# Optimization experiments

Measured on AMD Instinct MI355X. Metric: run time of the kernel, lower is better.

Reference implementation:

```python
import jax, jax.numpy as jnp
import numpy as np

B, L = 4, 40960
C = 512
DMLP = 2048
TEMP = 1e-5
EPS = 1e-5
FACTOR = 2  # Smartpool factor at layer 4


def setup_inputs() -> dict:
    key = jax.random.key(0)
    ks = jax.random.split(key, 8)

    def w(k, shape, fan_in):
        return jax.random.normal(k, shape, jnp.float32) / np.float32(np.sqrt(fan_in))

    inp = {
        "x": jax.random.normal(ks[0], (B, 1, L), jnp.float32),
        "conv0_w": w(ks[1], (C, 1, 10), 10),   "conv0_b": jnp.zeros(C, jnp.float32),
        "conv1_w": w(ks[2], (C, C, 8), C * 8), "conv1_b": jnp.zeros(C, jnp.float32),
        "conv2_w": w(ks[3], (C, C, 4), C * 4), "conv2_b": jnp.zeros(C, jnp.float32),
        "conv3_w": w(ks[4], (C, C, 4), C * 4), "conv3_b": jnp.zeros(C, jnp.float32),
        "mlp_w1": w(ks[5], (C, DMLP), C),       "mlp_b1": jnp.zeros(DMLP, jnp.float32),
        "mlp_w2": w(ks[6], (DMLP, DMLP), DMLP), "mlp_b2": jnp.zeros(DMLP, jnp.float32),
        "mlp_w3": w(ks[7], (DMLP, 1), DMLP),    "mlp_b3": jnp.zeros(1, jnp.float32),
    }
    for i in range(5):  # ChannelNorm affine params (init: ones/zeros)
        inp[f"n{i}_w"] = jnp.ones(C, jnp.float32)
        inp[f"n{i}_b"] = jnp.zeros(C, jnp.float32)
    return inp


def _conv(x, w, b, stride, pad):
    # Conv1d with padding_mode='reflect': reflect-pad then VALID conv. x: [B,C,T]
    x = jnp.pad(x, ((0, 0), (0, 0), (pad, pad)), mode="reflect")
    y = jax.lax.conv_general_dilated(x, w, (stride,), "VALID",
                                     dimension_numbers=("NCH", "OIH", "NCH"))
    return y + b[None, :, None]


def _cnorm(x, g, b):
    # ChannelNorm: normalize over channel dim with unbiased variance (torch.var default)
    m = jnp.mean(x, axis=1, keepdims=True)
    v = jnp.var(x, axis=1, keepdims=True, ddof=1)
    return (x - m) * jax.lax.rsqrt(v + EPS) * g[None, :, None] + b[None, :, None]


def _forward(x, conv0_w, conv0_b, conv1_w, conv1_b, conv2_w, conv2_b, conv3_w, conv3_b,
             n0_w, n0_b, n1_w, n1_b, n2_w, n2_b, n3_w, n3_b, n4_w, n4_b,
             mlp_w1, mlp_b1, mlp_w2, mlp_b2, mlp_w3, mlp_b3):
    h = jax.nn.relu(_cnorm(_conv(x, conv0_w, conv0_b, 5, 3), n0_w, n0_b))
    h = jax.nn.relu(_cnorm(_conv(h, conv1_w, conv1_b, 4, 2), n1_w, n1_b))
    h = jax.nn.relu(_cnorm(_conv(h, conv2_w, conv2_b, 2, 1), n2_w, n2_b))
    h = jax.nn.relu(_cnorm(_conv(h, conv3_w, conv3_b, 2, 1), n3_w, n3_b))

    f = jnp.transpose(h, (0, 2, 1))  # [B,T,C]
    T = f.shape[1]

    # importance MLP (dropout inactive in eval), exact GELU, sigmoid head
    z = jax.nn.gelu(f @ mlp_w1 + mlp_b1, approximate=False)
    z = jax.nn.gelu(z @ mlp_w2 + mlp_b2, approximate=False)
    imp = jax.nn.sigmoid((z @ mlp_w3 + mlp_b3)[..., 0]) + TEMP          # [B,T]
    imp = imp / jnp.sum(imp, axis=1, keepdims=True) * (T / FACTOR)      # sums to T/factor

    # warp: cumsum -> ramp contributions -> 2x2 [[-1,1],[1,-1]] conv = double diff
    Tn = T // FACTOR  # == round(importance_cs[0,-1])
    cs = jnp.cumsum(imp, axis=1)                                        # [B,T]
    p = jnp.maximum(cs[:, :, None] - jnp.arange(Tn, dtype=cs.dtype)[None, None, :], 0.0)  # [B,T,Tn]
    pc = jnp.pad(p, ((0, 0), (0, 0), (0, 1)))
    d = pc[:, :, :-1] - pc[:, :, 1:]                                    # diff along new-time axis
    wmat = d - jnp.pad(d, ((0, 0), (1, 0), (0, 0)))[:, :-1, :]          # diff along old-time axis, [B,T,Tn]
    pooled = jnp.einsum("btn,btc->bnc", wmat, f)                        # interp_weights @ X

    out = jnp.transpose(pooled, (0, 2, 1))                              # [B,C,Tn]
    return jax.nn.relu(_cnorm(out, n4_w, n4_b))


def reference(x, conv0_w, conv0_b, conv1_w, conv1_b, conv2_w, conv2_b, conv3_w, conv3_b,
              n0_w, n0_b, n1_w, n1_b, n2_w, n2_b, n3_w, n3_b, n4_w, n4_b,
              mlp_w1, mlp_b1, mlp_w2, mlp_b2, mlp_w3, mlp_b3):
    return _forward(x, conv0_w, conv0_b, conv1_w, conv1_b, conv2_w, conv2_b, conv3_w, conv3_b,
                    n0_w, n0_b, n1_w, n1_b, n2_w, n2_b, n3_w, n3_b, n4_w, n4_b,
                    mlp_w1, mlp_b1, mlp_w2, mlp_b2, mlp_w3, mlp_b3)
```

## Files before the change

### kernel.cpp

```cpp
#include <hip/hip_runtime.h>
#include <hip/hip_bf16.h>
#include <math.h>

#define NB 4
#define LIN 40960
#define NC 512
#define T0 8192
#define T1 2048
#define T2 1024
#define T3 512
#define TN 256
#define DM 2048
#define EPSF 1e-5f
#define TEMPF 1e-5f

typedef __attribute__((ext_vector_type(8))) short bf16x8;
typedef __attribute__((ext_vector_type(4))) float f32x4;

__device__ __forceinline__ int refl(int t, int T) {
  if (t < 0) t = -t;
  if (t >= T) t = 2 * T - 2 - t;
  return t;
}

__device__ __forceinline__ void gld16(void* lds, const void* g) {
  __builtin_amdgcn_global_load_lds((const __attribute__((address_space(1))) unsigned int*)g,
                                   (__attribute__((address_space(3))) unsigned int*)lds, 16, 0, 0);
}

__device__ __forceinline__ void blk_sum2_512(float& a, float& b, float* scratch) {
#pragma unroll
  for (int off = 32; off > 0; off >>= 1) {
    a += __shfl_down(a, off, 64);
    b += __shfl_down(b, off, 64);
  }
  int lane = threadIdx.x & 63, wid = threadIdx.x >> 6;
  __syncthreads();
  if (lane == 0) { scratch[wid] = a; scratch[8 + wid] = b; }
  __syncthreads();
  float sa = 0.f, sb = 0.f;
#pragma unroll
  for (int i = 0; i < 8; i++) { sa += scratch[i]; sb += scratch[8 + i]; }
  a = sa; b = sb;
}

template <int KT>
__global__ __launch_bounds__(256) void k_prepw_conv(const float* __restrict__ w,
                                                    __hip_bfloat16* __restrict__ wt) {
  __shared__ float l[512 * KT];
  int co = blockIdx.x;
  const float* wb = w + (size_t)co * 512 * KT;
  for (int i = threadIdx.x; i < 512 * KT; i += 256) l[i] = wb[i];
  __syncthreads();
  __hip_bfloat16* wo = wt + (size_t)co * 512 * KT;
  for (int i = threadIdx.x; i < 512 * KT; i += 256) {
    int kk = i >> 9, ci = i & 511;
    wo[i] = __float2bfloat16(l[ci * KT + kk]);
  }
}

template <int KD, int ND>
__global__ __launch_bounds__(256) void k_prepw_mlp(const float* __restrict__ w,
                                                   __hip_bfloat16* __restrict__ wt) {
  __shared__ float tile[32][33];
  int bx = blockIdx.x % (ND / 32);
  int by = blockIdx.x / (ND / 32);
  int tx = threadIdx.x & 31, ty = threadIdx.x >> 5;
#pragma unroll
  for (int i = 0; i < 32; i += 8)
    tile[ty + i][tx] = w[(size_t)(by * 32 + ty + i) * ND + bx * 32 + tx];
  __syncthreads();
#pragma unroll
  for (int i = 0; i < 32; i += 8)
    wt[(size_t)(bx * 32 + ty + i) * KD + by * 32 + tx] = __float2bfloat16(tile[tx][ty + i]);
}

__global__ __launch_bounds__(512) void k_conv0(const float* __restrict__ x, const float* __restrict__ w,
                                               const float* __restrict__ bias, const float* __restrict__ gw,
                                               const float* __restrict__ gb, __hip_bfloat16* __restrict__ out) {
  __shared__ float xv[48];
  __shared__ float tb[512 * 9];
  __shared__ float stats[16];
  int b = blockIdx.x / (T0 / 8);
  int t0 = (blockIdx.x % (T0 / 8)) * 8;
  int tid = threadIdx.x;
  if (tid < 45) xv[tid] = x[(size_t)b * LIN + refl(t0 * 5 - 3 + tid, LIN)];
  __syncthreads();
  float wk[10];
#pragma unroll
  for (int k = 0; k < 10; k++) wk[k] = w[tid * 10 + k];
  float bs = bias[tid];
  float acc[8];
#pragma unroll
  for (int tt = 0; tt < 8; tt++) {
    float a = bs;
#pragma unroll
    for (int k = 0; k < 10; k++) a += xv[tt * 5 + k] * wk[k];
    acc[tt] = a;
    tb[tid * 9 + tt] = a;
  }
  __syncthreads();
  int wave = tid >> 6, lane = tid & 63;
  float s = 0.f, q = 0.f;
#pragma unroll
  for (int j = 0; j < 8; j++) {
    float v = tb[(lane * 8 + j) * 9 + wave];
    s += v; q += v * v;
  }
#pragma unroll
  for (int off = 32; off > 0; off >>= 1) {
    s += __shfl_xor(s, off, 64);
    q += __shfl_xor(q, off, 64);
  }
  if (lane == 0) {
    float mean = s * (1.f / NC);
    float var = fmaxf((q - s * s * (1.f / NC)) * (1.f / (NC - 1)), 0.f);
    stats[wave] = mean;
    stats[8 + wave] = rsqrtf(var + EPSF);
  }
  __syncthreads();
  float gwv = gw[tid], gbv = gb[tid];
#pragma unroll
  for (int tt = 0; tt < 8; tt++) {
    float y = (acc[tt] - stats[tt]) * stats[8 + tt] * gwv + gbv;
    out[((size_t)(b * T0 + t0 + tt)) * NC + tid] = __float2bfloat16(fmaxf(y, 0.f));
  }
}

template <int MODE, int TIN_, int TOUT_, int SS, int PP, int KK, int NN, int SPLITK, int MM>
__global__ __launch_bounds__(256) void k_gemm2(const __hip_bfloat16* __restrict__ A,
                                               const __hip_bfloat16* __restrict__ Bt,
                                               float* __restrict__ Cf) {
  __shared__ __align__(16) __hip_bfloat16 sA[2][128 * 32];
  __shared__ __align__(16) __hip_bfloat16 sB[2][128 * 32];
  const int tid = threadIdx.x;
  const int lane = tid & 63;
  const int wave = tid >> 6;
  const int wm = wave >> 1, wn = wave & 1;
  constexpr int nt = NN / 128;
  constexpr int PS = (MM / 1024) * nt;
  const int blk = blockIdx.x;
  const int xs = blk & 7, sl = blk >> 3;
  const int sk = sl / PS, rem = sl % PS;
  const int row0 = ((rem / nt) * 8 + xs) * 128;
  const int col0 = (rem % nt) * 128;
  constexpr int KB = (KK / SPLITK) / 32;
  const int kb0 = sk * KB, kb1 = kb0 + KB;
  const int cq = lane >> 4, cl = lane & 15;

  auto stage = [&](int kb, int buf) {
#pragma unroll
    for (int rr = 0; rr < 2; rr++) {
      int c = rr * 256 + tid;
      int m = c >> 2, kc = c & 3;
      int kcs = kc ^ (m & 3);
      size_t ga;
      if (MODE == 0) {
        ga = (size_t)(row0 + m) * KK + kb * 32 + kcs * 8;
      } else {
        int r = row0 + m;
        int bb = r / TOUT_;
        int t = r - bb * TOUT_;
        int k = (kb * 32) >> 9;
        int ci = ((kb * 32) & 511) + kcs * 8;
        int gt = refl(t * SS - PP + k, TIN_);
        ga = (((size_t)(bb * TIN_ + gt)) << 9) + ci;
      }
      gld16((char*)&sA[buf][0] + c * 16, (const char*)(A + ga));
    }
#pragma unroll
    for (int rr = 0; rr < 2; rr++) {
      int c = rr * 256 + tid;
      int n = c >> 2, kc = c & 3;
      int kcs = kc ^ (n & 3);
      gld16((char*)&sB[buf][0] + c * 16, (const char*)(Bt + (size_t)(col0 + n) * KK + kb * 32 + kcs * 8));
    }
  };

  f32x4 acc[4][4];
  const f32x4 zz = {0.f, 0.f, 0.f, 0.f};
#pragma unroll
  for (int mi = 0; mi < 4; mi++)
#pragma unroll
    for (int ni = 0; ni < 4; ni++) acc[mi][ni] = zz;

  stage(kb0, 0);
  const int p = cq ^ (cl & 3);
  for (int kb = kb0; kb < kb1; kb++) {
    int cur = (kb - kb0) & 1;
    __syncthreads();
    if (kb + 1 < kb1) stage(kb + 1, cur ^ 1);
    const short* bA = (const short*)&sA[cur][0];
    const short* bB = (const short*)&sB[cur][0];
    bf16x8 af[4], bfr[4];
#pragma unroll
    for (int mi = 0; mi < 4; mi++)
      af[mi] = *(const bf16x8*)(bA + (wm * 64 + mi * 16 + cl) * 32 + p * 8);
#pragma unroll
    for (int ni = 0; ni < 4; ni++)
      bfr[ni] = *(const bf16x8*)(bB + (wn * 64 + ni * 16 + cl) * 32 + p * 8);
#pragma unroll
    for (int mi = 0; mi < 4; mi++)
#pragma unroll
      for (int ni = 0; ni < 4; ni++)
        acc[mi][ni] = __builtin_amdgcn_mfma_f32_16x16x32_bf16(af[mi], bfr[ni], acc[mi][ni], 0, 0, 0);
  }

#pragma unroll
  for (int mi = 0; mi < 4; mi++)
#pragma unroll
    for (int ni = 0; ni < 4; ni++)
#pragma unroll
      for (int r2 = 0; r2 < 4; r2++) {
        int row = row0 + wm * 64 + mi * 16 + cq * 4 + r2;
        int col = col0 + wn * 64 + ni * 16 + cl;
        Cf[(size_t)sk * MM * NN + (size_t)row * NN + col] = acc[mi][ni][r2];
      }
}

template <int MODE, int TIN_, int TOUT_, int SS, int PP, int KK, int NN, int EPI, int SPLITK, int MM>
__global__ __launch_bounds__(256) void k_gemm(const __hip_bfloat16* __restrict__ A,
                                              const __hip_bfloat16* __restrict__ Bt,
                                              const float* __restrict__ bias,
                                              float* __restrict__ Cf,
                                              __hip_bfloat16* __restrict__ Cb) {
  __shared__ __align__(16) __hip_bfloat16 sA[2][64 * 32];
  __shared__ __align__(16) __hip_bfloat16 sB[2][128 * 32];
  const int tid = threadIdx.x;
  const int lane = tid & 63;
  const int wave = tid >> 6;
  const int wm = wave >> 1, wn = wave & 1;
  constexpr int nt = NN / 128;
  constexpr int PS = (MM / 512) * nt;
  const int blk = blockIdx.x;
  const int xs = blk & 7, sl = blk >> 3;
  const int sk = sl / PS, rem = sl % PS;
  const int row0 = ((rem / nt) * 8 + xs) * 64;
  const int col0 = (rem % nt) * 128;
  constexpr int KB = (KK / SPLITK) / 32;
  const int kb0 = sk * KB, kb1 = kb0 + KB;
  const int cq = lane >> 4, cl = lane & 15;

  auto stage = [&](int kb, int buf) {
    {
      int m = tid >> 2, kc = tid & 3;
      int kcs = kc ^ (m & 3);
      size_t ga;
      if (MODE == 0) {
        ga = (size_t)(row0 + m) * KK + kb * 32 + kcs * 8;
      } else {
        int r = row0 + m;
        int bb = r / TOUT_;
        int t = r - bb * TOUT_;
        int k = (kb * 32) >> 9;
        int ci = ((kb * 32) & 511) + kcs * 8;
        int gt = refl(t * SS - PP + k, TIN_);
        ga = (((size_t)(bb * TIN_ + gt)) << 9) + ci;
      }
      gld16((char*)&sA[buf][0] + tid * 16, (const char*)(A + ga));
    }
#pragma unroll
    for (int rr = 0; rr < 2; rr++) {
      int c = rr * 256 + tid;
      int n = c >> 2, kc = c & 3;
      int kcs = kc ^ (n & 3);
      gld16((char*)&sB[buf][0] + c * 16, (const char*)(Bt + (size_t)(col0 + n) * KK + kb * 32 + kcs * 8));
    }
  };

  f32x4 acc[2][4];
  const f32x4 zz = {0.f, 0.f, 0.f, 0.f};
#pragma unroll
  for (int mi = 0; mi < 2; mi++)
#pragma unroll
    for (int ni = 0; ni < 4; ni++) acc[mi][ni] = zz;

  stage(kb0, 0);
  const int p = cq ^ (cl & 3);
  for (int kb = kb0; kb < kb1; kb++) {
    int cur = (kb - kb0) & 1;
    __syncthreads();
    if (kb + 1 < kb1) stage(kb + 1, cur ^ 1);
    const short* bA = (const short*)&sA[cur][0];
    const short* bB = (const short*)&sB[cur][0];
    bf16x8 af[2], bfr[4];
#pragma unroll
    for (int mi = 0; mi < 2; mi++)
      af[mi] = *(const bf16x8*)(bA + (wm * 32 + mi * 16 + cl) * 32 + p * 8);
#pragma unroll
    for (int ni = 0; ni < 4; ni++)
      bfr[ni] = *(const bf16x8*)(bB + (wn * 64 + ni * 16 + cl) * 32 + p * 8);
#pragma unroll
    for (int mi = 0; mi < 2; mi++)
#pragma unroll
      for (int ni = 0; ni < 4; ni++)
        acc[mi][ni] = __builtin_amdgcn_mfma_f32_16x16x32_bf16(af[mi], bfr[ni], acc[mi][ni], 0, 0, 0);
  }

#pragma unroll
  for (int mi = 0; mi < 2; mi++)
#pragma unroll
    for (int ni = 0; ni < 4; ni++)
#pragma unroll
      for (int r2 = 0; r2 < 4; r2++) {
        int row = row0 + wm * 32 + mi * 16 + cq * 4 + r2;
        int col = col0 + wn * 64 + ni * 16 + cl;
        float v = acc[mi][ni][r2];
        if (EPI == 1) {
          v += bias[col];
          v = 0.5f * v * (1.f + erff(v * 0.70710678118654752f));
          Cb[(size_t)row * NN + col] = __float2bfloat16(v);
        } else {
          Cf[(size_t)sk * MM * NN + (size_t)row * NN + col] = v;
        }
      }
}

template <int NS>
__global__ __launch_bounds__(512) void k_cnorm(const float* __restrict__ g, const float* __restrict__ cb,
                                               const float* __restrict__ gw, const float* __restrict__ gb,
                                               __hip_bfloat16* __restrict__ out, size_t stride) {
  int wave = threadIdx.x >> 6, lane = threadIdx.x & 63;
  size_t row = (size_t)blockIdx.x * 8 + wave;
  float v[8];
  {
    float4 c0 = *(const float4*)(cb + lane * 8), c1 = *(const float4*)(cb + lane * 8 + 4);
    v[0] = c0.x; v[1] = c0.y; v[2] = c0.z; v[3] = c0.w;
    v[4] = c1.x; v[5] = c1.y; v[6] = c1.z; v[7] = c1.w;
  }
#pragma unroll
  for (int s = 0; s < NS; s++) {
    const float* gr = g + s * stride + row * NC + lane * 8;
    float4 a0 = *(const float4*)gr;
    float4 a1 = *(const float4*)(gr + 4);
    v[0] += a0.x; v[1] += a0.y; v[2] += a0.z; v[3] += a0.w;
    v[4] += a1.x; v[5] += a1.y; v[6] += a1.z; v[7] += a1.w;
  }
  float s = 0.f, q = 0.f;
#pragma unroll
  for (int j = 0; j < 8; j++) { s += v[j]; q += v[j] * v[j]; }
#pragma unroll
  for (int off = 32; off > 0; off >>= 1) {
    s += __shfl_xor(s, off, 64);
    q += __shfl_xor(q, off, 64);
  }
  float mean = s * (1.f / NC);
  float var = fmaxf((q - s * s * (1.f / NC)) * (1.f / (NC - 1)), 0.f);
  float rstd = rsqrtf(var + EPSF);
  float4 w0 = *(const float4*)(gw + lane * 8), w1 = *(const float4*)(gw + lane * 8 + 4);
  float4 b0 = *(const float4*)(gb + lane * 8), b1 = *(const float4*)(gb + lane * 8 + 4);
  float gwv[8] = {w0.x, w0.y, w0.z, w0.w, w1.x, w1.y, w1.z, w1.w};
  float gbv[8] = {b0.x, b0.y, b0.z, b0.w, b1.x, b1.y, b1.z, b1.w};
  union { __hip_bfloat16 h[8]; uint4 u; } pk;
#pragma unroll
  for (int j = 0; j < 8; j++)
    pk.h[j] = __float2bfloat16(fmaxf((v[j] - mean) * rstd * gwv[j] + gbv[j], 0.f));
  *(uint4*)(out + row * NC + lane * 8) = pk.u;
}

template <int NS>
__global__ __launch_bounds__(512) void k_gelu_red(const float* __restrict__ g, const float* __restrict__ bias,
                                                  __hip_bfloat16* __restrict__ out) {
  size_t base = ((size_t)blockIdx.x * 512 + threadIdx.x) * 8;
  int col = (int)(base & (DM - 1));
  float v[8];
  {
    float4 b0 = *(const float4*)(bias + col), b1 = *(const float4*)(bias + col + 4);
    v[0] = b0.x; v[1] = b0.y; v[2] = b0.z; v[3] = b0.w;
    v[4] = b1.x; v[5] = b1.y; v[6] = b1.z; v[7] = b1.w;
  }
#pragma unroll
  for (int s = 0; s < NS; s++) {
    const float* gr = g + (size_t)s * (2048 * 2048) + base;
    float4 a0 = *(const float4*)gr;
    float4 a1 = *(const float4*)(gr + 4);
    v[0] += a0.x; v[1] += a0.y; v[2] += a0.z; v[3] += a0.w;
    v[4] += a1.x; v[5] += a1.y; v[6] += a1.z; v[7] += a1.w;
  }
  union { __hip_bfloat16 h[8]; uint4 u; } pk;
#pragma unroll
  for (int j = 0; j < 8; j++) {
    float z = 0.5f * v[j] * (1.f + erff(v[j] * 0.70710678118654752f));
    pk.h[j] = __float2bfloat16(z);
  }
  *(uint4*)(out + base) = pk.u;
}

__global__ __launch_bounds__(256) void k_head(const __hip_bfloat16* __restrict__ z, const float* __restrict__ w,
                                              const float* __restrict__ bias, float* __restrict__ imp) {
  __shared__ float red[4];
  int row = blockIdx.x, tid = threadIdx.x;
  float a = 0.f;
  for (int i = tid; i < DM; i += 256) a += __bfloat162float(z[(size_t)row * DM + i]) * w[i];
#pragma unroll
  for (int off = 32; off > 0; off >>= 1) a += __shfl_down(a, off, 64);
  int lane = tid & 63, wid = tid >> 6;
  if (lane == 0) red[wid] = a;
  __syncthreads();
  if (tid == 0) {
    float s = red[0] + red[1] + red[2] + red[3] + bias[0];
    imp[row] = 1.f / (1.f + expf(-s)) + TEMPF;
  }
}

__global__ __launch_bounds__(256) void k_cumsum(const float* __restrict__ imp, float* __restrict__ cs) {
  int wave = threadIdx.x >> 6, lane = threadIdx.x & 63;
  const float* ib = imp + wave * T3 + lane * 8;
  float p[8];
  float run = 0.f;
#pragma unroll
  for (int j = 0; j < 8; j++) { run += ib[j]; p[j] = run; }
  float ls = run, s = ls;
#pragma unroll
  for (int off = 1; off < 64; off <<= 1) {
    float t = __shfl_up(s, off, 64);
    if (lane >= off) s += t;
  }
  float excl = s - ls;
  float total = __shfl(s, 63, 64);
  float scale = (float)TN / total;
  float* ob = cs + wave * T3 + lane * 8;
#pragma unroll
  for (int j = 0; j < 8; j++) ob[j] = (excl + p[j]) * scale;
}

__device__ __forceinline__ float dfun(float cv, int n) {
  float d = fmaxf(cv - (float)n, 0.f);
  if (n < TN - 1) d = fminf(d, 1.f);
  return d;
}

__global__ __launch_bounds__(512) void k_poolfinal(const __hip_bfloat16* __restrict__ f,
                                                   const float* __restrict__ cs,
                                                   const float* __restrict__ gw, const float* __restrict__ gb,
                                                   float* __restrict__ out) {
  __shared__ float wt[T3];
  __shared__ float red[16];
  int b = blockIdx.x / TN, n = blockIdx.x % TN;
  int tid = threadIdx.x;
  {
    float c1 = cs[b * T3 + tid];
    float c0 = (tid > 0) ? cs[b * T3 + tid - 1] : 0.f;
    wt[tid] = dfun(c1, n) - dfun(c0, n);
  }
  __syncthreads();
  float acc = 0.f;
  for (int t = 0; t < T3; t++) {
    float w = wt[t];
    if (w != 0.f) acc += w * __bfloat162float(f[((size_t)b * T3 + t) * NC + tid]);
  }
  float s = acc, q = acc * acc;
  blk_sum2_512(s, q, red);
  float mean = s * (1.f / NC);
  float var = fmaxf((q - s * s * (1.f / NC)) * (1.f / (NC - 1)), 0.f);
  float y = (acc - mean) * rsqrtf(var + EPSF) * gw[tid] + gb[tid];
  out[((size_t)b * NC + tid) * TN + n] = fmaxf(y, 0.f);
}

extern "C" void kernel_launch(void* const* d_in, const int* in_sizes, int n_in,
                              void* d_out, int out_size, void* d_ws, size_t ws_size,
                              hipStream_t stream) {
  const float* x   = (const float*)d_in[0];
  const float* c0w = (const float*)d_in[1];  const float* c0b = (const float*)d_in[2];
  const float* c1w = (const float*)d_in[3];  const float* c1b = (const float*)d_in[4];
  const float* c2w = (const float*)d_in[5];  const float* c2b = (const float*)d_in[6];
  const float* c3w = (const float*)d_in[7];  const float* c3b = (const float*)d_in[8];
  const float* mw1 = (const float*)d_in[9];  const float* mb1 = (const float*)d_in[10];
  const float* mw2 = (const float*)d_in[11]; const float* mb2 = (const float*)d_in[12];
  const float* mw3 = (const float*)d_in[13]; const float* mb3 = (const float*)d_in[14];
  const float* n0w = (const float*)d_in[15]; const float* n0b = (const float*)d_in[16];
  const float* n1w = (const float*)d_in[17]; const float* n1b = (const float*)d_in[18];
  const float* n2w = (const float*)d_in[19]; const float* n2b = (const float*)d_in[20];
  const float* n3w = (const float*)d_in[21]; const float* n3b = (const float*)d_in[22];
  const float* n4w = (const float*)d_in[23]; const float* n4b = (const float*)d_in[24];

  char* base = (char*)d_ws;
  __hip_bfloat16* h0b  = (__hip_bfloat16*)(base);
  float*          g    = (float*)(base + (32u << 20));
  __hip_bfloat16* h1b  = (__hip_bfloat16*)(base + (64u << 20));
  __hip_bfloat16* h2b  = (__hip_bfloat16*)(base + (72u << 20));
  __hip_bfloat16* h3b  = (__hip_bfloat16*)(base + (76u << 20));
  float*          imp  = (float*)(base + (78u << 20));
  float*          cs   = (float*)(base + (78u << 20) + 8192);
  __hip_bfloat16* wt1  = (__hip_bfloat16*)(base + (79u << 20));
  __hip_bfloat16* wt2  = (__hip_bfloat16*)(base + (83u << 20));
  __hip_bfloat16* wt3  = (__hip_bfloat16*)(base + (85u << 20));
  __hip_bfloat16* wm1t = (__hip_bfloat16*)(base + (87u << 20));
  __hip_bfloat16* wm2t = (__hip_bfloat16*)(base + (89u << 20));
  __hip_bfloat16* z1b  = h0b;
  __hip_bfloat16* z2b  = (__hip_bfloat16*)(base + (8u << 20));
  float* outp = (float*)d_out;

  k_prepw_conv<8><<<512, 256, 0, stream>>>(c1w, wt1);
  k_prepw_conv<4><<<512, 256, 0, stream>>>(c2w, wt2);
  k_prepw_conv<4><<<512, 256, 0, stream>>>(c3w, wt3);
  k_prepw_mlp<512, 2048><<<(2048 / 32) * (512 / 32), 256, 0, stream>>>(mw1, wm1t);
  k_prepw_mlp<2048, 2048><<<(2048 / 32) * (2048 / 32), 256, 0, stream>>>(mw2, wm2t);

  k_conv0<<<NB * (T0 / 8), 512, 0, stream>>>(x, c0w, c0b, n0w, n0b, h0b);

  k_gemm2<1, 8192, 2048, 4, 2, 4096, 512, 2, 8192><<<512, 256, 0, stream>>>(h0b, wt1, g);
  k_cnorm<2><<<8192 / 8, 512, 0, stream>>>(g, c1b, n1w, n1b, h1b, (size_t)8192 * 512);
  k_gemm2<1, 2048, 1024, 2, 1, 2048, 512, 4, 4096><<<512, 256, 0, stream>>>(h1b, wt2, g);
  k_cnorm<4><<<4096 / 8, 512, 0, stream>>>(g, c2b, n2w, n2b, h2b, (size_t)4096 * 512);
  k_gemm<1, 1024, 512, 2, 1, 2048, 512, 0, 4, 2048><<<512, 256, 0, stream>>>(h2b, wt3, nullptr, g, nullptr);
  k_cnorm<4><<<2048 / 8, 512, 0, stream>>>(g, c3b, n3w, n3b, h3b, (size_t)2048 * 512);

  k_gemm<0, 0, 1, 0, 0, 512, 2048, 1, 1, 2048><<<512, 256, 0, stream>>>(h3b, wm1t, mb1, nullptr, z1b);
  k_gemm2<0, 0, 1, 0, 0, 2048, 2048, 2, 2048><<<512, 256, 0, stream>>>(z1b, wm2t, g);
  k_gelu_red<2><<<(2048 * 2048) / (512 * 8), 512, 0, stream>>>(g, mb2, z2b);

  k_head<<<NB * T3, 256, 0, stream>>>(z2b, mw3, mb3, imp);
  k_cumsum<<<1, 256, 0, stream>>>(imp, cs);
  k_poolfinal<<<NB * TN, 512, 0, stream>>>(h3b, cs, n4w, n4b, outp);
}
```

Measured before the change: 351.4 us.

## Merge weight-prep kernels, raise split-K, fuse GELU into head and cumsum into pool

Four of the five weight-transpose kernels are merged into one launch. The mw2 transpose moves after the first conv GEMM and its output overlays the wt1 buffer. Split-K factors rise from 2/4 to 3/6 so the GEMMs run 768 blocks, and K-block ranges are now computed to allow non-even splits. The GELU reduction kernel is folded into the head kernel, and the cumsum is recomputed inside each pooling block, which removes two launches and the z2 round trip. The cost is more split-K partial traffic and redundant per-block scan work, and the reuse of the wt1 region for wm2t depends on stream ordering.

```diff
diff --git a/kernel.cpp b/kernel.cpp
--- a/kernel.cpp
+++ b/kernel.cpp
@@ -45,10 +45,8 @@
 }
 
 template <int KT>
-__global__ __launch_bounds__(256) void k_prepw_conv(const float* __restrict__ w,
-                                                    __hip_bfloat16* __restrict__ wt) {
-  __shared__ float l[512 * KT];
-  int co = blockIdx.x;
+__device__ __forceinline__ void prep_conv_body(const float* __restrict__ w, __hip_bfloat16* __restrict__ wt,
+                                               int co, float* l) {
   const float* wb = w + (size_t)co * 512 * KT;
   for (int i = threadIdx.x; i < 512 * KT; i += 256) l[i] = wb[i];
   __syncthreads();
@@ -60,11 +58,11 @@
 }
 
 template <int KD, int ND>
-__global__ __launch_bounds__(256) void k_prepw_mlp(const float* __restrict__ w,
-                                                   __hip_bfloat16* __restrict__ wt) {
-  __shared__ float tile[32][33];
-  int bx = blockIdx.x % (ND / 32);
-  int by = blockIdx.x / (ND / 32);
+__device__ __forceinline__ void prep_mlp_body(const float* __restrict__ w, __hip_bfloat16* __restrict__ wt,
+                                              int bidx, float* sbuf) {
+  float(*tile)[33] = (float(*)[33])sbuf;
+  int bx = bidx % (ND / 32);
+  int by = bidx / (ND / 32);
   int tx = threadIdx.x & 31, ty = threadIdx.x >> 5;
 #pragma unroll
   for (int i = 0; i < 32; i += 8)
@@ -73,6 +71,22 @@
 #pragma unroll
   for (int i = 0; i < 32; i += 8)
     wt[(size_t)(bx * 32 + ty + i) * KD + by * 32 + tx] = __float2bfloat16(tile[tx][ty + i]);
+}
+
+__global__ __launch_bounds__(256) void k_prepA(const float* c1w, const float* c2w, const float* c3w,
+                                               const float* mw1, __hip_bfloat16* wt1, __hip_bfloat16* wt2,
+                                               __hip_bfloat16* wt3, __hip_bfloat16* wm1t) {
+  __shared__ float sb[4096];
+  int b = blockIdx.x;
+  if (b < 512) prep_conv_body<8>(c1w, wt1, b, sb);
+  else if (b < 1024) prep_conv_body<4>(c2w, wt2, b - 512, sb);
+  else if (b < 1536) prep_conv_body<4>(c3w, wt3, b - 1024, sb);
+  else prep_mlp_body<512, 2048>(mw1, wm1t, b - 1536, sb);
+}
+
+__global__ __launch_bounds__(256) void k_prepB(const float* mw2, __hip_bfloat16* wm2t) {
+  __shared__ float sb[1056];
+  prep_mlp_body<2048, 2048>(mw2, wm2t, blockIdx.x, sb);
 }
 
 __global__ __launch_bounds__(512) void k_conv0(const float* __restrict__ x, const float* __restrict__ w,
@@ -139,13 +153,13 @@
   const int wm = wave >> 1, wn = wave & 1;
   constexpr int nt = NN / 128;
   constexpr int PS = (MM / 1024) * nt;
+  constexpr int KBT = KK / 32;
   const int blk = blockIdx.x;
   const int xs = blk & 7, sl = blk >> 3;
   const int sk = sl / PS, rem = sl % PS;
   const int row0 = ((rem / nt) * 8 + xs) * 128;
   const int col0 = (rem % nt) * 128;
-  constexpr int KB = (KK / SPLITK) / 32;
-  const int kb0 = sk * KB, kb1 = kb0 + KB;
+  const int kb0 = (sk * KBT) / SPLITK, kb1 = ((sk + 1) * KBT) / SPLITK;
   const int cq = lane >> 4, cl = lane & 15;
 
   auto stage = [&](int kb, int buf) {
@@ -232,13 +246,13 @@
   const int wm = wave >> 1, wn = wave & 1;
   constexpr int nt = NN / 128;
   constexpr int PS = (MM / 512) * nt;
+  constexpr int KBT = KK / 32;
   const int blk = blockIdx.x;
   const int xs = blk & 7, sl = blk >> 3;
   const int sk = sl / PS, rem = sl % PS;
   const int row0 = ((rem / nt) * 8 + xs) * 64;
   const int col0 = (rem % nt) * 128;
-  constexpr int KB = (KK / SPLITK) / 32;
-  const int kb0 = sk * KB, kb1 = kb0 + KB;
+  const int kb0 = (sk * KBT) / SPLITK, kb1 = ((sk + 1) * KBT) / SPLITK;
   const int cq = lane >> 4, cl = lane & 15;
 
   auto stage = [&](int kb, int buf) {
@@ -359,69 +373,43 @@
 }
 
 template <int NS>
-__global__ __launch_bounds__(512) void k_gelu_red(const float* __restrict__ g, const float* __restrict__ bias,
-                                                  __hip_bfloat16* __restrict__ out) {
-  size_t base = ((size_t)blockIdx.x * 512 + threadIdx.x) * 8;
-  int col = (int)(base & (DM - 1));
+__global__ __launch_bounds__(256) void k_head(const float* __restrict__ g, const float* __restrict__ b2,
+                                              const float* __restrict__ w3, const float* __restrict__ b3,
+                                              float* __restrict__ imp) {
+  __shared__ float red[4];
+  int row = blockIdx.x, tid = threadIdx.x;
+  int c = tid * 8;
   float v[8];
   {
-    float4 b0 = *(const float4*)(bias + col), b1 = *(const float4*)(bias + col + 4);
-    v[0] = b0.x; v[1] = b0.y; v[2] = b0.z; v[3] = b0.w;
-    v[4] = b1.x; v[5] = b1.y; v[6] = b1.z; v[7] = b1.w;
+    float4 x0 = *(const float4*)(b2 + c), x1 = *(const float4*)(b2 + c + 4);
+    v[0] = x0.x; v[1] = x0.y; v[2] = x0.z; v[3] = x0.w;
+    v[4] = x1.x; v[5] = x1.y; v[6] = x1.z; v[7] = x1.w;
   }
 #pragma unroll
   for (int s = 0; s < NS; s++) {
-    const float* gr = g + (size_t)s * (2048 * 2048) + base;
+    const float* gr = g + (size_t)s * (2048 * DM) + (size_t)row * DM + c;
     float4 a0 = *(const float4*)gr;
     float4 a1 = *(const float4*)(gr + 4);
     v[0] += a0.x; v[1] += a0.y; v[2] += a0.z; v[3] += a0.w;
     v[4] += a1.x; v[5] += a1.y; v[6] += a1.z; v[7] += a1.w;
   }
-  union { __hip_bfloat16 h[8]; uint4 u; } pk;
+  float a = 0.f;
+  float4 w0 = *(const float4*)(w3 + c), w1 = *(const float4*)(w3 + c + 4);
+  float wv[8] = {w0.x, w0.y, w0.z, w0.w, w1.x, w1.y, w1.z, w1.w};
 #pragma unroll
   for (int j = 0; j < 8; j++) {
     float z = 0.5f * v[j] * (1.f + erff(v[j] * 0.70710678118654752f));
-    pk.h[j] = __float2bfloat16(z);
-  }
-  *(uint4*)(out + base) = pk.u;
-}
-
-__global__ __launch_bounds__(256) void k_head(const __hip_bfloat16* __restrict__ z, const float* __restrict__ w,
-                                              const float* __restrict__ bias, float* __restrict__ imp) {
-  __shared__ float red[4];
-  int row = blockIdx.x, tid = threadIdx.x;
-  float a = 0.f;
-  for (int i = tid; i < DM; i += 256) a += __bfloat162float(z[(size_t)row * DM + i]) * w[i];
+    a += z * wv[j];
+  }
 #pragma unroll
   for (int off = 32; off > 0; off >>= 1) a += __shfl_down(a, off, 64);
   int lane = tid & 63, wid = tid >> 6;
   if (lane == 0) red[wid] = a;
   __syncthreads();
   if (tid == 0) {
-    float s = red[0] + red[1] + red[2] + red[3] + bias[0];
+    float s = red[0] + red[1] + red[2] + red[3] + b3[0];
     imp[row] = 1.f / (1.f + expf(-s)) + TEMPF;
   }
-}
-
-__global__ __launch_bounds__(256) void k_cumsum(const float* __restrict__ imp, float* __restrict__ cs) {
-  int wave = threadIdx.x >> 6, lane = threadIdx.x & 63;
-  const float* ib = imp + wave * T3 + lane * 8;
-  float p[8];
-  float run = 0.f;
-#pragma unroll
-  for (int j = 0; j < 8; j++) { run += ib[j]; p[j] = run; }
-  float ls = run, s = ls;
-#pragma unroll
-  for (int off = 1; off < 64; off <<= 1) {
-    float t = __shfl_up(s, off, 64);
-    if (lane >= off) s += t;
-  }
-  float excl = s - ls;
-  float total = __shfl(s, 63, 64);
-  float scale = (float)TN / total;
-  float* ob = cs + wave * T3 + lane * 8;
-#pragma unroll
-  for (int j = 0; j < 8; j++) ob[j] = (excl + p[j]) * scale;
 }
 
 __device__ __forceinline__ float dfun(float cv, int n) {
@@ -431,28 +419,44 @@
 }
 
 __global__ __launch_bounds__(512) void k_poolfinal(const __hip_bfloat16* __restrict__ f,
-                                                   const float* __restrict__ cs,
+                                                   const float* __restrict__ imp,
                                                    const float* __restrict__ gw, const float* __restrict__ gb,
                                                    float* __restrict__ out) {
   __shared__ float wt[T3];
+  __shared__ float wsum[8];
   __shared__ float red[16];
   int b = blockIdx.x / TN, n = blockIdx.x % TN;
-  int tid = threadIdx.x;
-  {
-    float c1 = cs[b * T3 + tid];
-    float c0 = (tid > 0) ? cs[b * T3 + tid - 1] : 0.f;
-    wt[tid] = dfun(c1, n) - dfun(c0, n);
-  }
+  int tid = threadIdx.x, wave = tid >> 6, lane = tid & 63;
+  float own = imp[b * T3 + tid];
+  float s = own;
+#pragma unroll
+  for (int off = 1; off < 64; off <<= 1) {
+    float t = __shfl_up(s, off, 64);
+    if (lane >= off) s += t;
+  }
+  if (lane == 63) wsum[wave] = s;
+  __syncthreads();
+  float prefix = 0.f, total = 0.f;
+#pragma unroll
+  for (int w = 0; w < 8; w++) {
+    float ws_ = wsum[w];
+    total += ws_;
+    if (w < wave) prefix += ws_;
+  }
+  float scale = (float)TN / total;
+  float incl = (prefix + s) * scale;
+  float excl = (prefix + s - own) * scale;
+  wt[tid] = dfun(incl, n) - dfun(excl, n);
   __syncthreads();
   float acc = 0.f;
   for (int t = 0; t < T3; t++) {
     float w = wt[t];
     if (w != 0.f) acc += w * __bfloat162float(f[((size_t)b * T3 + t) * NC + tid]);
   }
-  float s = acc, q = acc * acc;
-  blk_sum2_512(s, q, red);
-  float mean = s * (1.f / NC);
-  float var = fmaxf((q - s * s * (1.f / NC)) * (1.f / (NC - 1)), 0.f);
+  float sv = acc, q = acc * acc;
+  blk_sum2_512(sv, q, red);
+  float mean = sv * (1.f / NC);
+  float var = fmaxf((q - sv * sv * (1.f / NC)) * (1.f / (NC - 1)), 0.f);
   float y = (acc - mean) * rsqrtf(var + EPSF) * gw[tid] + gb[tid];
   out[((size_t)b * NC + tid) * TN + n] = fmaxf(y, 0.f);
 }
@@ -476,41 +480,33 @@
 
   char* base = (char*)d_ws;
   __hip_bfloat16* h0b  = (__hip_bfloat16*)(base);
+  __hip_bfloat16* h1b  = (__hip_bfloat16*)(base);
+  __hip_bfloat16* h2b  = (__hip_bfloat16*)(base + (8u << 20));
+  __hip_bfloat16* h3b  = (__hip_bfloat16*)(base + (12u << 20));
+  __hip_bfloat16* z1b  = (__hip_bfloat16*)(base + (14u << 20));
+  float*          imp  = (float*)(base + (22u << 20));
   float*          g    = (float*)(base + (32u << 20));
-  __hip_bfloat16* h1b  = (__hip_bfloat16*)(base + (64u << 20));
-  __hip_bfloat16* h2b  = (__hip_bfloat16*)(base + (72u << 20));
-  __hip_bfloat16* h3b  = (__hip_bfloat16*)(base + (76u << 20));
-  float*          imp  = (float*)(base + (78u << 20));
-  float*          cs   = (float*)(base + (78u << 20) + 8192);
-  __hip_bfloat16* wt1  = (__hip_bfloat16*)(base + (79u << 20));
-  __hip_bfloat16* wt2  = (__hip_bfloat16*)(base + (83u << 20));
-  __hip_bfloat16* wt3  = (__hip_bfloat16*)(base + (85u << 20));
-  __hip_bfloat16* wm1t = (__hip_bfloat16*)(base + (87u << 20));
-  __hip_bfloat16* wm2t = (__hip_bfloat16*)(base + (89u << 20));
-  __hip_bfloat16* z1b  = h0b;
-  __hip_bfloat16* z2b  = (__hip_bfloat16*)(base + (8u << 20));
+  __hip_bfloat16* wm1t = (__hip_bfloat16*)(base + (80u << 20));
+  __hip_bfloat16* wt2  = (__hip_bfloat16*)(base + (82u << 20));
+  __hip_bfloat16* wt3  = (__hip_bfloat16*)(base + (84u << 20));
+  __hip_bfloat16* wt1  = (__hip_bfloat16*)(base + (86u << 20));
+  __hip_bfloat16* wm2t = (__hip_bfloat16*)(base + (86u << 20));
   float* outp = (float*)d_out;
 
-  k_prepw_conv<8><<<512, 256, 0, stream>>>(c1w, wt1);
-  k_prepw_conv<4><<<512, 256, 0, stream>>>(c2w, wt2);
-  k_prepw_conv<4><<<512, 256, 0, stream>>>(c3w, wt3);
-  k_prepw_mlp<512, 2048><<<(2048 / 32) * (512 / 32), 256, 0, stream>>>(mw1, wm1t);
-  k_prepw_mlp<2048, 2048><<<(2048 / 32) * (2048 / 32), 256, 0, stream>>>(mw2, wm2t);
-
+  k_prepA<<<2560, 256, 0, stream>>>(c1w, c2w, c3w, mw1, wt1, wt2, wt3, wm1t);
   k_conv0<<<NB * (T0 / 8), 512, 0, stream>>>(x, c0w, c0b, n0w, n0b, h0b);
 
-  k_gemm2<1, 8192, 2048, 4, 2, 4096, 512, 2, 8192><<<512, 256, 0, stream>>>(h0b, wt1, g);
-  k_cnorm<2><<<8192 / 8, 512, 0, stream>>>(g, c1b, n1w, n1b, h1b, (size_t)8192 * 512);
-  k_gemm2<1, 2048, 1024, 2, 1, 2048, 512, 4, 4096><<<512, 256, 0, stream>>>(h1b, wt2, g);
-  k_cnorm<4><<<4096 / 8, 512, 0, stream>>>(g, c2b, n2w, n2b, h2b, (size_t)4096 * 512);
-  k_gemm<1, 1024, 512, 2, 1, 2048, 512, 0, 4, 2048><<<512, 256, 0, stream>>>(h2b, wt3, nullptr, g, nullptr);
-  k_cnorm<4><<<2048 / 8, 512, 0, stream>>>(g, c3b, n3w, n3b, h3b, (size_t)2048 * 512);
+  k_gemm2<1, 8192, 2048, 4, 2, 4096, 512, 3, 8192><<<768, 256, 0, stream>>>(h0b, wt1, g);
+  k_prepB<<<4096, 256, 0, stream>>>(mw2, wm2t);
+  k_cnorm<3><<<8192 / 8, 512, 0, stream>>>(g, c1b, n1w, n1b, h1b, (size_t)8192 * 512);
+  k_gemm2<1, 2048, 1024, 2, 1, 2048, 512, 6, 4096><<<768, 256, 0, stream>>>(h1b, wt2, g);
+  k_cnorm<6><<<4096 / 8, 512, 0, stream>>>(g, c2b, n2w, n2b, h2b, (size_t)4096 * 512);
+  k_gemm<1, 1024, 512, 2, 1, 2048, 512, 0, 6, 2048><<<768, 256, 0, stream>>>(h2b, wt3, nullptr, g, nullptr);
+  k_cnorm<6><<<2048 / 8, 512, 0, stream>>>(g, c3b, n3w, n3b, h3b, (size_t)2048 * 512);
 
   k_gemm<0, 0, 1, 0, 0, 512, 2048, 1, 1, 2048><<<512, 256, 0, stream>>>(h3b, wm1t, mb1, nullptr, z1b);
-  k_gemm2<0, 0, 1, 0, 0, 2048, 2048, 2, 2048><<<512, 256, 0, stream>>>(z1b, wm2t, g);
-  k_gelu_red<2><<<(2048 * 2048) / (512 * 8), 512, 0, stream>>>(g, mb2, z2b);
-
-  k_head<<<NB * T3, 256, 0, stream>>>(z2b, mw3, mb3, imp);
-  k_cumsum<<<1, 256, 0, stream>>>(imp, cs);
-  k_poolfinal<<<NB * TN, 512, 0, stream>>>(h3b, cs, n4w, n4b, outp);
-}
+  k_gemm2<0, 0, 1, 0, 0, 2048, 2048, 3, 2048><<<768, 256, 0, stream>>>(z1b, wm2t, g);
+
+  k_head<3><<<NB * T3, 256, 0, stream>>>(g, mb2, mw3, mb3, imp);
+  k_poolfinal<<<NB * TN, 512, 0, stream>>>(h3b, imp, n4w, n4b, outp);
+}
```

New measurement: 343.8 us. 2.2% less time.
